# Kernel tuning notes

Hardware: AMD Instinct MI355X
Metric: run time of the kernel (lower is better)

Reference implementation:

```python
import jax, jax.numpy as jnp
import numpy as np

N = 50000   # nodes
E = 600000  # edges (avg degree 12)
D = 128     # feature dim (input_dim == output_dim for residual)
G = 8       # graphs in batch
EPS = 1e-5


def setup_inputs() -> dict:
    key = jax.random.key(0)
    ks = jax.random.split(key, 8)
    x = jax.random.normal(ks[0], (N, D), dtype=jnp.float32)
    edge_index = jax.random.randint(ks[1], (2, E), 0, N)
    batch = jnp.sort(jax.random.randint(ks[2], (N,), 0, G))
    s = 1.0 / np.sqrt(D)
    Wl = jax.random.normal(ks[3], (D, D), dtype=jnp.float32) * s
    bl = jax.random.normal(ks[4], (D,), dtype=jnp.float32) * s
    Wr = jax.random.normal(ks[5], (D, D), dtype=jnp.float32) * s
    return {
        "x": x,
        "edge_index": edge_index,
        "batch": batch,
        "num_graphs": G,
        "Wl": Wl,
        "bl": bl,
        "Wr": Wr,
        "gn_weight": jnp.ones((D,), jnp.float32),
        "gn_bias": jnp.zeros((D,), jnp.float32),
        "mean_scale": jnp.ones((D,), jnp.float32),
    }


def reference(x, edge_index, batch, num_graphs, Wl, bl, Wr, gn_weight, gn_bias, mean_scale):
    n = x.shape[0]
    src, dst = edge_index[0], edge_index[1]

    # SAGEConv: mean-aggregate neighbor (source) features at target nodes
    ones_e = jnp.ones(src.shape[0], dtype=x.dtype)
    deg = jax.ops.segment_sum(ones_e, dst, num_segments=n)          # [N]
    agg = jax.ops.segment_sum(x[src], dst, num_segments=n)          # [N, D]
    agg = agg / jnp.maximum(deg, 1.0)[:, None]
    f = agg @ Wl.T + bl + x @ Wr.T                                  # lin_l(agg) + lin_r(x)

    # exact (erf) GELU, as torch F.gelu default
    f = jax.nn.gelu(f, approximate=False)

    # GraphNorm: per-graph statistics with learnable mean_scale
    ones_n = jnp.ones(n, dtype=x.dtype)
    cnt = jax.ops.segment_sum(ones_n, batch, num_segments=num_graphs)[:, None]  # [G,1]
    mean = jax.ops.segment_sum(f, batch, num_segments=num_graphs) / cnt         # [G,D]
    out = f - mean_scale * mean[batch]
    var = jax.ops.segment_sum(out * out, batch, num_segments=num_graphs) / cnt  # [G,D]
    out = out / jnp.sqrt(var[batch] + EPS) * gn_weight + gn_bias

    # dropout is identity in eval mode; residual add
    return out + x
```

## Files before the change

### kernel.cpp

```cpp
#include <hip/hip_runtime.h>

#define D 128
#define NGRAPH 8
#define EPS 1e-5f
#define CAP 48

typedef __attribute__((ext_vector_type(4))) float f32x4;
typedef __attribute__((ext_vector_type(8))) short s16x8;

__device__ __forceinline__ unsigned short f2bf(float f) {
    unsigned int u = __float_as_uint(f);
    u += 0x7fffu + ((u >> 16) & 1u);
    return (unsigned short)(u >> 16);
}
__device__ __forceinline__ float blo(unsigned int u) { return __uint_as_float(u << 16); }
__device__ __forceinline__ float bhi(unsigned int u) { return __uint_as_float(u & 0xffff0000u); }

__global__ __launch_bounds__(256) void prep_fill_kernel(
    const float* __restrict__ Wl, const float* __restrict__ Wr,
    unsigned short* __restrict__ Bsw,
    const float* __restrict__ x, unsigned int* __restrict__ xb,
    const int* __restrict__ batch, int* __restrict__ bnd,
    const int* __restrict__ ei, int* __restrict__ cnt, int* __restrict__ adj,
    int N, int E, int Npad, int fillB)
{
    int b = blockIdx.x;
    if (b < 128) {
        int t = b * 256 + threadIdx.x;
        int j    = t & 7;
        int ln   = (t >> 3) & 63;
        int ks   = (t >> 9) & 7;
        int tile = t >> 12;
        int k = ks * 32 + (ln >> 4) * 8 + j;
        int d = tile * 16 + (ln & 15);
        float v = (k < 128) ? Wl[(size_t)d * 128 + k] : Wr[(size_t)d * 128 + (k - 128)];
        Bsw[t] = f2bf(v);
    } else if (b == 128) {
        int g = threadIdx.x;
        if (g <= NGRAPH) {
            int lo = 0, hi = N;
            while (lo < hi) {
                int mid = (lo + hi) >> 1;
                if (batch[mid] < g) lo = mid + 1; else hi = mid;
            }
            bnd[g] = lo;
        }
    } else if (b < 129 + fillB) {
        int e = (b - 129) * 256 + threadIdx.x;
        if (e < E) {
            int dst = ei[E + e];
            int pos = atomicAdd(&cnt[dst], 1);
            if (pos < CAP) adj[(size_t)dst * CAP + pos] = ei[e];
        }
    } else {
        int iu = (b - 129 - fillB) * 256 + threadIdx.x;
        if (iu < N * 32) {
            float4 p = *(const float4*)(x + (size_t)iu * 4);
            uint2 o;
            o.x = (unsigned int)f2bf(p.x) | ((unsigned int)f2bf(p.y) << 16);
            o.y = (unsigned int)f2bf(p.z) | ((unsigned int)f2bf(p.w) << 16);
            *(uint2*)(xb + (size_t)iu * 2) = o;
        } else if (iu < Npad * 32) {
            *(uint2*)(xb + (size_t)iu * 2) = make_uint2(0u, 0u);
        }
    }
}

template<int COOP>
__global__ __launch_bounds__(256, 4) void fused_kernel(
    const unsigned int* __restrict__ xb, const int* __restrict__ cnt,
    const int* __restrict__ adj, const unsigned short* __restrict__ Bsw,
    const float* __restrict__ bl, const int* __restrict__ batch,
    const int* __restrict__ bnd, const float* __restrict__ x,
    const float* __restrict__ ms, const float* __restrict__ gw,
    const float* __restrict__ gb,
    float* __restrict__ gsum, float* __restrict__ gsumsq,
    unsigned int* __restrict__ bar, float* __restrict__ fout,
    float* __restrict__ out, int N)
{
    __shared__ unsigned int aggL[64][68];

    int wave = threadIdx.x >> 6, lane = threadIdx.x & 63;
    int row0 = blockIdx.x * 64 + wave * 16;
    int m = lane & 15, quad = lane >> 4;
    int r = row0 + m;
    int lrow = wave * 16;

    for (int mm = 0; mm < 16; ++mm) {
        int node = row0 + mm;
        int dg = (node < N) ? cnt[node] : 0;
        int lm = dg < CAP ? dg : CAP;
        int idxv = (lane < lm) ? adj[(size_t)node * CAP + lane] : 0;
        float a0 = 0.0f, a1 = 0.0f;
        int i = 0;
        for (; i + 8 <= lm; i += 8) {
            int nb[8];
#pragma unroll
            for (int k = 0; k < 8; ++k) nb[k] = __shfl(idxv, i + k, 64);
            unsigned int u[8];
#pragma unroll
            for (int k = 0; k < 8; ++k) u[k] = xb[(size_t)nb[k] * 64 + lane];
#pragma unroll
            for (int k = 0; k < 8; ++k) { a0 += blo(u[k]); a1 += bhi(u[k]); }
        }
        for (; i < lm; ++i) {
            int nb = __shfl(idxv, i, 64);
            unsigned int u = xb[(size_t)nb * 64 + lane];
            a0 += blo(u); a1 += bhi(u);
        }
        float iv = 1.0f / (float)(dg > 0 ? dg : 1);
        aggL[lrow + mm][lane] =
            (unsigned int)f2bf(a0 * iv) | ((unsigned int)f2bf(a1 * iv) << 16);
    }

    s16x8 afrag[8];
#pragma unroll
    for (int ks = 0; ks < 4; ++ks)
        afrag[ks] = *(const s16x8*)&aggL[lrow + m][ks * 16 + quad * 4];
    const unsigned short* xp = (const unsigned short*)xb + (size_t)r * 128 + quad * 8;
#pragma unroll
    for (int ks = 0; ks < 4; ++ks) afrag[4 + ks] = *(const s16x8*)(xp + ks * 32);

    int nbase = row0;
    bool uni = (nbase + 15 < N) && (batch[nbase] == batch[nbase + 15]);
    int gu = (nbase < N) ? batch[nbase] : 0;

    float val[8][4];
#pragma unroll
    for (int tile = 0; tile < 8; ++tile) {
        f32x4 acc = {0.0f, 0.0f, 0.0f, 0.0f};
        const s16x8* bptr = (const s16x8*)Bsw + (size_t)(tile * 8) * 64 + lane;
#pragma unroll
        for (int ks = 0; ks < 8; ++ks)
            acc = __builtin_amdgcn_mfma_f32_16x16x32_bf16(afrag[ks], bptr[(size_t)ks * 64], acc, 0, 0, 0);
        int d = tile * 16 + m;
        float bias = bl[d];
        float sm = 0.0f, sq = 0.0f;
#pragma unroll
        for (int rr = 0; rr < 4; ++rr) {
            int node = nbase + quad * 4 + rr;
            float v = acc[rr] + bias;
            float g = 0.5f * v * (1.0f + erff(v * 0.70710678118654752f));
            val[tile][rr] = g;
            if (node < N) {
                if (uni) { sm += g; sq += g * g; }
                else {
                    int gg = batch[node];
                    unsafeAtomicAdd(&gsum[gg * D + d], g);
                    unsafeAtomicAdd(&gsumsq[gg * D + d], g * g);
                }
            }
        }
        if (uni) {
            sm += __shfl_xor(sm, 16, 64); sm += __shfl_xor(sm, 32, 64);
            sq += __shfl_xor(sq, 16, 64); sq += __shfl_xor(sq, 32, 64);
            if (quad == 0) {
                unsafeAtomicAdd(&gsum[gu * D + d], sm);
                unsafeAtomicAdd(&gsumsq[gu * D + d], sq);
            }
        }
    }

    if constexpr (!COOP) {
#pragma unroll
        for (int tile = 0; tile < 8; ++tile) {
            int d = tile * 16 + m;
#pragma unroll
            for (int rr = 0; rr < 4; ++rr) {
                int node = nbase + quad * 4 + rr;
                if (node < N) fout[(size_t)node * D + d] = val[tile][rr];
            }
        }
        return;
    }

    __syncthreads();
    if (threadIdx.x == 0) {
        __hip_atomic_fetch_add(bar, 1u, __ATOMIC_ACQ_REL, __HIP_MEMORY_SCOPE_AGENT);
        unsigned long long t0 = __builtin_amdgcn_s_memrealtime();
        while (__hip_atomic_load(bar, __ATOMIC_RELAXED, __HIP_MEMORY_SCOPE_AGENT) < gridDim.x) {
            __builtin_amdgcn_s_sleep(10);
            if (__builtin_amdgcn_s_memrealtime() - t0 > 5000000ull) break;
        }
    }
    __syncthreads();

    int node0 = nbase + quad * 4;
    if (node0 < N) {
        int last = (node0 + 3 < N - 1) ? node0 + 3 : N - 1;
        int g0 = batch[node0];
        int gL = batch[last];
        if (g0 == gL) {
            int c = bnd[g0 + 1] - bnd[g0];
            float invc = 1.0f / (float)(c > 0 ? c : 1);
#pragma unroll
            for (int tile = 0; tile < 8; ++tile) {
                int d = tile * 16 + m;
                float s1 = __hip_atomic_load(&gsum[g0 * D + d], __ATOMIC_RELAXED, __HIP_MEMORY_SCOPE_AGENT);
                float s2 = __hip_atomic_load(&gsumsq[g0 * D + d], __ATOMIC_RELAXED, __HIP_MEMORY_SCOPE_AGENT);
                float mu = s1 * invc, q = s2 * invc, a = ms[d] * mu;
                float sc = rsqrtf(q - 2.0f * a * mu + a * a + EPS);
                float gwv = gw[d], gbv = gb[d];
#pragma unroll
                for (int rr = 0; rr < 4; ++rr) {
                    int node = node0 + rr;
                    if (node < N)
                        out[(size_t)node * D + d] =
                            (val[tile][rr] - a) * sc * gwv + gbv + x[(size_t)node * D + d];
                }
            }
        } else {
#pragma unroll
            for (int rr = 0; rr < 4; ++rr) {
                int node = node0 + rr;
                if (node >= N) continue;
                int g = batch[node];
                int c = bnd[g + 1] - bnd[g];
                float invc = 1.0f / (float)(c > 0 ? c : 1);
#pragma unroll
                for (int tile = 0; tile < 8; ++tile) {
                    int d = tile * 16 + m;
                    float s1 = __hip_atomic_load(&gsum[g * D + d], __ATOMIC_RELAXED, __HIP_MEMORY_SCOPE_AGENT);
                    float s2 = __hip_atomic_load(&gsumsq[g * D + d], __ATOMIC_RELAXED, __HIP_MEMORY_SCOPE_AGENT);
                    float mu = s1 * invc, q = s2 * invc, a = ms[d] * mu;
                    float sc = rsqrtf(q - 2.0f * a * mu + a * a + EPS);
                    out[(size_t)node * D + d] =
                        (val[tile][rr] - a) * sc * gw[d] + gb[d] + x[(size_t)node * D + d];
                }
            }
        }
    }
}

__global__ __launch_bounds__(256) void final_kernel(
    const float* __restrict__ f, const float* __restrict__ x,
    const int* __restrict__ batch, const int* __restrict__ bnd,
    const float* __restrict__ gsum, const float* __restrict__ gsumsq,
    const float* __restrict__ ms,
    const float* __restrict__ gw, const float* __restrict__ gb,
    float* __restrict__ out, int N)
{
    int t = blockIdx.x * 256 + threadIdx.x;
    if (t >= N * (D / 4)) return;
    int n  = t >> 5;
    int d0 = (t & 31) * 4;
    int g  = batch[n];
    int c  = bnd[g + 1] - bnd[g];
    float invc = 1.0f / (float)(c > 0 ? c : 1);
    size_t row = (size_t)n * D + d0;
    float4 fv = *(const float4*)(f + row);
    float4 xv = *(const float4*)(x + row);
    float4 s1 = *(const float4*)(gsum + g * D + d0);
    float4 s2 = *(const float4*)(gsumsq + g * D + d0);
    float4 msv = *(const float4*)(ms + d0);
    float4 gwv = *(const float4*)(gw + d0);
    float4 gbv = *(const float4*)(gb + d0);
    float4 o;
    {
        float mu = s1.x * invc, q = s2.x * invc, a = msv.x * mu;
        float sc = rsqrtf(q - 2.0f * a * mu + a * a + EPS);
        o.x = (fv.x - a) * sc * gwv.x + gbv.x + xv.x;
    }
    {
        float mu = s1.y * invc, q = s2.y * invc, a = msv.y * mu;
        float sc = rsqrtf(q - 2.0f * a * mu + a * a + EPS);
        o.y = (fv.y - a) * sc * gwv.y + gbv.y + xv.y;
    }
    {
        float mu = s1.z * invc, q = s2.z * invc, a = msv.z * mu;
        float sc = rsqrtf(q - 2.0f * a * mu + a * a + EPS);
        o.z = (fv.z - a) * sc * gwv.z + gbv.z + xv.z;
    }
    {
        float mu = s1.w * invc, q = s2.w * invc, a = msv.w * mu;
        float sc = rsqrtf(q - 2.0f * a * mu + a * a + EPS);
        o.w = (fv.w - a) * sc * gwv.w + gbv.w + xv.w;
    }
    *(float4*)(out + row) = o;
}

extern "C" void kernel_launch(void* const* d_in, const int* in_sizes, int n_in,
                              void* d_out, int out_size, void* d_ws, size_t ws_size,
                              hipStream_t stream)
{
    const float* x     = (const float*)d_in[0];
    const int*   ei    = (const int*)d_in[1];
    const int*   batch = (const int*)d_in[2];
    const float* Wl = (const float*)d_in[4];
    const float* bl = (const float*)d_in[5];
    const float* Wr = (const float*)d_in[6];
    const float* gw = (const float*)d_in[7];
    const float* gb = (const float*)d_in[8];
    const float* ms = (const float*)d_in[9];
    float* out = (float*)d_out;

    int N = in_sizes[0] / D;
    int E = in_sizes[1] / 2;
    int NBLK = (N + 63) / 64;
    int Npad = NBLK * 64;

    float*          fout = (float*)d_ws;
    unsigned int*   xb   = (unsigned int*)(fout + (size_t)Npad * D);
    unsigned short* Bsw  = (unsigned short*)(xb + (size_t)Npad * 64);
    float* gsum   = (float*)(Bsw + 32768);
    float* gsumsq = gsum + NGRAPH * D;
    unsigned int* bar = (unsigned int*)(gsumsq + NGRAPH * D);
    int*   cnt    = (int*)(bar + 4);
    int*   bnd    = cnt + N;
    int*   adj    = bnd + (NGRAPH + 1);

    hipMemsetAsync(gsum, 0,
                   (2 * NGRAPH * D) * sizeof(float) + 4 * sizeof(unsigned int)
                   + (size_t)N * sizeof(int), stream);

    int fillB = (E + 255) / 256;
    int xbB   = (Npad * 32 + 255) / 256;
    prep_fill_kernel<<<129 + fillB + xbB, 256, 0, stream>>>(
        Wl, Wr, Bsw, x, xb, batch, bnd, ei, cnt, adj, N, E, Npad, fillB);

    int occ = 0, ncu = 0, dev = 0;
    bool coop = false;
    if (hipOccupancyMaxActiveBlocksPerMultiprocessor(&occ, fused_kernel<1>, 256, 0) == hipSuccess) {
        if (hipGetDevice(&dev) != hipSuccess) dev = 0;
        if (hipDeviceGetAttribute(&ncu, hipDeviceAttributeMultiprocessorCount, dev) != hipSuccess || ncu <= 0)
            ncu = 256;
        coop = ((long long)occ * (long long)ncu >= (long long)NBLK);
    }

    if (coop) {
        fused_kernel<1><<<NBLK, 256, 0, stream>>>(
            xb, cnt, adj, Bsw, bl, batch, bnd, x, ms, gw, gb,
            gsum, gsumsq, bar, fout, out, N);
    } else {
        fused_kernel<0><<<NBLK, 256, 0, stream>>>(
            xb, cnt, adj, Bsw, bl, batch, bnd, x, ms, gw, gb,
            gsum, gsumsq, bar, fout, out, N);
        int threads = N * (D / 4);
        final_kernel<<<(threads + 255) / 256, 256, 0, stream>>>(
            fout, x, batch, bnd, gsum, gsumsq, ms, gw, gb, out, N);
    }
}
```

Measured before the change: 207.3 us.

## Split neighbor aggregation into a separate wide-grid kernel before fused GEMM

Moves the gather-mean aggregation out of the fused GEMM kernel into its own kernel that assigns one wave per node over a grid of Npad/4 blocks. The fused kernel then loads aggregated bf16 rows straight from global memory instead of going through a shared-memory staging tile. This is meant to give the latency-bound gather many more waves in flight than the limited cooperative grid allows, and to shorten the fused kernel before its grid barrier. In exchange it adds a kernel launch and a global round trip for the N×128 bf16 aggregate buffer, and it places that buffer after the adjacency array in the workspace, which assumes the workspace is large enough.

```diff
diff --git a/kernel.cpp b/kernel.cpp
--- a/kernel.cpp
+++ b/kernel.cpp
@@ -66,58 +66,61 @@
     }
 }
 
+__global__ __launch_bounds__(256) void aggregate_kernel(
+    const unsigned int* __restrict__ xb, const int* __restrict__ cnt,
+    const int* __restrict__ adj, unsigned int* __restrict__ Aag, int N, int Npad)
+{
+    int n = blockIdx.x * 4 + (threadIdx.x >> 6);
+    int lane = threadIdx.x & 63;
+    if (n >= Npad) return;
+    if (n >= N) { Aag[(size_t)n * 64 + lane] = 0u; return; }
+    int deg = cnt[n];
+    int lim = deg < CAP ? deg : CAP;
+    int v = (lane < lim) ? adj[(size_t)n * CAP + lane] : 0;
+    float a0 = 0.0f, a1 = 0.0f;
+    int i = 0;
+    for (; i + 8 <= lim; i += 8) {
+        int nb[8];
+#pragma unroll
+        for (int k = 0; k < 8; ++k) nb[k] = __shfl(v, i + k, 64);
+        unsigned int u[8];
+#pragma unroll
+        for (int k = 0; k < 8; ++k) u[k] = xb[(size_t)nb[k] * 64 + lane];
+#pragma unroll
+        for (int k = 0; k < 8; ++k) { a0 += blo(u[k]); a1 += bhi(u[k]); }
+    }
+    for (; i < lim; ++i) {
+        int nb = __shfl(v, i, 64);
+        unsigned int u = xb[(size_t)nb * 64 + lane];
+        a0 += blo(u); a1 += bhi(u);
+    }
+    float inv = 1.0f / (float)(deg > 0 ? deg : 1);
+    Aag[(size_t)n * 64 + lane] =
+        (unsigned int)f2bf(a0 * inv) | ((unsigned int)f2bf(a1 * inv) << 16);
+}
+
 template<int COOP>
 __global__ __launch_bounds__(256, 4) void fused_kernel(
-    const unsigned int* __restrict__ xb, const int* __restrict__ cnt,
-    const int* __restrict__ adj, const unsigned short* __restrict__ Bsw,
-    const float* __restrict__ bl, const int* __restrict__ batch,
-    const int* __restrict__ bnd, const float* __restrict__ x,
+    const unsigned short* __restrict__ Aag, const unsigned short* __restrict__ xb16,
+    const unsigned short* __restrict__ Bsw, const float* __restrict__ bl,
+    const int* __restrict__ batch, const int* __restrict__ bnd,
+    const float* __restrict__ x,
     const float* __restrict__ ms, const float* __restrict__ gw,
     const float* __restrict__ gb,
     float* __restrict__ gsum, float* __restrict__ gsumsq,
     unsigned int* __restrict__ bar, float* __restrict__ fout,
     float* __restrict__ out, int N)
 {
-    __shared__ unsigned int aggL[64][68];
-
     int wave = threadIdx.x >> 6, lane = threadIdx.x & 63;
     int row0 = blockIdx.x * 64 + wave * 16;
     int m = lane & 15, quad = lane >> 4;
     int r = row0 + m;
-    int lrow = wave * 16;
-
-    for (int mm = 0; mm < 16; ++mm) {
-        int node = row0 + mm;
-        int dg = (node < N) ? cnt[node] : 0;
-        int lm = dg < CAP ? dg : CAP;
-        int idxv = (lane < lm) ? adj[(size_t)node * CAP + lane] : 0;
-        float a0 = 0.0f, a1 = 0.0f;
-        int i = 0;
-        for (; i + 8 <= lm; i += 8) {
-            int nb[8];
-#pragma unroll
-            for (int k = 0; k < 8; ++k) nb[k] = __shfl(idxv, i + k, 64);
-            unsigned int u[8];
-#pragma unroll
-            for (int k = 0; k < 8; ++k) u[k] = xb[(size_t)nb[k] * 64 + lane];
-#pragma unroll
-            for (int k = 0; k < 8; ++k) { a0 += blo(u[k]); a1 += bhi(u[k]); }
-        }
-        for (; i < lm; ++i) {
-            int nb = __shfl(idxv, i, 64);
-            unsigned int u = xb[(size_t)nb * 64 + lane];
-            a0 += blo(u); a1 += bhi(u);
-        }
-        float iv = 1.0f / (float)(dg > 0 ? dg : 1);
-        aggL[lrow + mm][lane] =
-            (unsigned int)f2bf(a0 * iv) | ((unsigned int)f2bf(a1 * iv) << 16);
-    }
 
     s16x8 afrag[8];
-#pragma unroll
-    for (int ks = 0; ks < 4; ++ks)
-        afrag[ks] = *(const s16x8*)&aggL[lrow + m][ks * 16 + quad * 4];
-    const unsigned short* xp = (const unsigned short*)xb + (size_t)r * 128 + quad * 8;
+    const unsigned short* ab = Aag + (size_t)r * 128 + quad * 8;
+#pragma unroll
+    for (int ks = 0; ks < 4; ++ks) afrag[ks] = *(const s16x8*)(ab + ks * 32);
+    const unsigned short* xp = xb16 + (size_t)r * 128 + quad * 8;
 #pragma unroll
     for (int ks = 0; ks < 4; ++ks) afrag[4 + ks] = *(const s16x8*)(xp + ks * 32);
 
@@ -308,6 +311,7 @@
     int*   cnt    = (int*)(bar + 4);
     int*   bnd    = cnt + N;
     int*   adj    = bnd + (NGRAPH + 1);
+    unsigned int* Aag = (unsigned int*)(adj + (size_t)N * CAP);
 
     hipMemsetAsync(gsum, 0,
                    (2 * NGRAPH * D) * sizeof(float) + 4 * sizeof(unsigned int)
@@ -317,6 +321,8 @@
     int xbB   = (Npad * 32 + 255) / 256;
     prep_fill_kernel<<<129 + fillB + xbB, 256, 0, stream>>>(
         Wl, Wr, Bsw, x, xb, batch, bnd, ei, cnt, adj, N, E, Npad, fillB);
+
+    aggregate_kernel<<<Npad / 4, 256, 0, stream>>>(xb, cnt, adj, Aag, N, Npad);
 
     int occ = 0, ncu = 0, dev = 0;
     bool coop = false;
@@ -329,12 +335,12 @@
 
     if (coop) {
         fused_kernel<1><<<NBLK, 256, 0, stream>>>(
-            xb, cnt, adj, Bsw, bl, batch, bnd, x, ms, gw, gb,
-            gsum, gsumsq, bar, fout, out, N);
+            (const unsigned short*)Aag, (const unsigned short*)xb, Bsw, bl,
+            batch, bnd, x, ms, gw, gb, gsum, gsumsq, bar, fout, out, N);
     } else {
         fused_kernel<0><<<NBLK, 256, 0, stream>>>(
-            xb, cnt, adj, Bsw, bl, batch, bnd, x, ms, gw, gb,
-            gsum, gsumsq, bar, fout, out, N);
+            (const unsigned short*)Aag, (const unsigned short*)xb, Bsw, bl,
+            batch, bnd, x, ms, gw, gb, gsum, gsumsq, bar, fout, out, N);
         int threads = N * (D / 4);
         final_kernel<<<(threads + 255) / 256, 256, 0, stream>>>(
             fout, x, batch, bnd, gsum, gsumsq, ms, gw, gb, out, N);
```

Result: no change. 203.7 us (-1.7%).
